# Kernel tuning notes

Measured on AMD Instinct MI355X. Metric: run time of the kernel, lower is better.

Reference implementation:

```python
import jax, jax.numpy as jnp
import numpy as np

N = 50000       # nodes
E = 800000      # edges (before self-loops)
F_IN = 128      # in_channels
HID = 32        # hidden_channels per head
HEADS = 4
OUT = 16        # out_channels
NEG_SLOPE = 0.2 # PyG GATConv leaky_relu slope
EPS = 1e-16     # PyG softmax denominator eps
BN_EPS = 1e-5


def setup_inputs() -> dict:
    key = jax.random.key(0)
    ks = jax.random.split(key, 20)
    rn = lambda k, shp, s=0.1: (jax.random.normal(k, shp, jnp.float32) * s)
    x = jax.random.normal(ks[0], (N, F_IN), jnp.float32)
    edge_index = jax.random.randint(ks[1], (2, E), 0, N, dtype=jnp.int32)
    D0 = HEADS * HID  # 128
    return {
        "x": x, "edge_index": edge_index,
        # layer 0: GATConv(F_IN -> HID, heads=HEADS, concat=True)
        "W0": rn(ks[2], (F_IN, HEADS * HID)), "as0": rn(ks[3], (HEADS, HID)),
        "ad0": rn(ks[4], (HEADS, HID)), "b0": jnp.zeros((D0,), jnp.float32),
        "g0": jnp.ones((D0,), jnp.float32) + rn(ks[5], (D0,), 0.05),
        "be0": rn(ks[6], (D0,), 0.05),
        # layer 1: GATConv(D0 -> HID, heads=HEADS, concat=True)
        "W1": rn(ks[7], (D0, HEADS * HID)), "as1": rn(ks[8], (HEADS, HID)),
        "ad1": rn(ks[9], (HEADS, HID)), "b1": jnp.zeros((D0,), jnp.float32),
        "g1": jnp.ones((D0,), jnp.float32) + rn(ks[10], (D0,), 0.05),
        "be1": rn(ks[11], (D0,), 0.05),
        # layer 2: GATConv(D0 -> OUT, heads=1, concat=False)
        "W2": rn(ks[12], (D0, OUT)), "as2": rn(ks[13], (1, OUT)),
        "ad2": rn(ks[14], (1, OUT)), "b2": jnp.zeros((OUT,), jnp.float32),
    }


def _gat(x, src, dst, W, a_s, a_d, b, heads, ch, concat):
    n = x.shape[0]
    h = (x @ W).reshape(n, heads, ch)                       # [N,H,C]
    score_s = (h * a_s).sum(-1)                             # [N,H]
    score_d = (h * a_d).sum(-1)                             # [N,H]
    e = jax.nn.leaky_relu(score_s[src] + score_d[dst], NEG_SLOPE)  # [E,H]
    emax = jax.ops.segment_max(e, dst, num_segments=n)
    emax = jnp.where(jnp.isfinite(emax), emax, 0.0)
    p = jnp.exp(e - emax[dst])
    denom = jax.ops.segment_sum(p, dst, num_segments=n)
    alpha = p / (denom[dst] + EPS)                          # segment softmax over dst
    out = jax.ops.segment_sum(h[src] * alpha[:, :, None], dst, num_segments=n)
    out = out.reshape(n, heads * ch) if concat else out.mean(axis=1)
    return out + b


def _bn(x, g, be):
    m = x.mean(0)
    v = x.var(0)
    return (x - m) * jax.lax.rsqrt(v + BN_EPS) * g + be


def reference(x, edge_index, W0, as0, ad0, b0, g0, be0,
              W1, as1, ad1, b1, g1, be1, W2, as2, ad2, b2):
    n = x.shape[0]
    loop = jnp.arange(n, dtype=edge_index.dtype)
    src = jnp.concatenate([edge_index[0], loop])  # PyG add_self_loops
    dst = jnp.concatenate([edge_index[1], loop])
    h = _gat(x, src, dst, W0, as0, ad0, b0, HEADS, HID, True)
    h = jax.nn.elu(_bn(h, g0, be0))                 # dropout disabled (eval)
    h = _gat(h, src, dst, W1, as1, ad1, b1, HEADS, HID, True)
    h = jax.nn.elu(_bn(h, g1, be1))
    return _gat(h, src, dst, W2, as2, ad2, b2, 1, OUT, False)
```

## Files before the change

kernel.cpp:

```cpp
#include <hip/hip_runtime.h>
#include <hip/hip_bf16.h>
#include <math.h>

#define NEG_SLOPE 0.2f
#define EPS_SM 1e-16f
#define BN_EPS 1e-5f
#define RANK_BLOCKS 256

typedef __attribute__((ext_vector_type(8))) short bf16x8;
typedef __attribute__((ext_vector_type(4))) float f32x4;

__device__ __forceinline__ float lrelu(float x) { return x > 0.f ? x : NEG_SLOPE * x; }
__device__ __forceinline__ ushort f2bf(float f) {
    uint u = __float_as_uint(f);
    return (ushort)((u + 0x7FFFu + ((u >> 16) & 1u)) >> 16);
}
__device__ __forceinline__ float bfl(uint u) { return __uint_as_float(u << 16); }
__device__ __forceinline__ float bfh(uint u) { return __uint_as_float(u & 0xFFFF0000u); }

__global__ void pack_w(const float* __restrict__ W0, const float* __restrict__ W1,
                       const float* __restrict__ W2, ushort* __restrict__ P0,
                       ushort* __restrict__ P1, ushort* __restrict__ P2) {
    int i = blockIdx.x * blockDim.x + threadIdx.x;
    const float* W;
    ushort* P;
    int NC, s;
    if (i < 16384) { W = W0; P = P0; NC = 128; s = i; }
    else if (i < 32768) { W = W1; P = P1; NC = 128; s = i - 16384; }
    else if (i < 34816) { W = W2; P = P2; NC = 16; s = i - 32768; }
    else return;
    int k = s / NC, col = s % NC;
    int CT = NC >> 4;
    int dst = (((k >> 5) * CT + (col >> 4)) << 9) +
              (((col & 15) | (((k >> 3) & 3) << 4)) << 3) + (k & 7);
    P[dst] = f2bf(W[s]);
}

template <int NC, bool BNELU, int HEADS, bool RANKFUSE>
__global__ __launch_bounds__(256) void gemm_mfma(
    const float* __restrict__ X, const ushort* __restrict__ Wp, ushort* __restrict__ Hb, int n,
    const float* __restrict__ sumsP, const float* __restrict__ g, const float* __restrict__ be,
    const float* __restrict__ as_, const float* __restrict__ ad_,
    float* __restrict__ ss, float* __restrict__ sd,
    const int* __restrict__ dstE, int E, int* __restrict__ deg, ushort* __restrict__ rank) {
    int tid = threadIdx.x;
    if constexpr (RANKFUSE) {
        if ((int)blockIdx.x < RANK_BLOCKS) {
            int T = RANK_BLOCKS * 256;
            for (int i = (int)blockIdx.x * 256 + tid; i < E; i += T)
                rank[i] = (ushort)atomicAdd(&deg[dstE[i]], 1);
            return;
        }
    }
    constexpr int CT = NC / 16;
    constexpr int FPH = NC / HEADS / 16;
    __shared__ __align__(16) ushort Xb[64 * 128];
    int bid = RANKFUSE ? ((int)blockIdx.x - RANK_BLOCKS) : (int)blockIdx.x;
    int row0 = bid * 64;
    float bnM[4], bnS[4], bnB[4];
    if constexpr (BNELU) {
        int c0 = (tid & 31) * 4;
        float inv_n = 1.f / (float)n;
#pragma unroll
        for (int j = 0; j < 4; ++j) {
            float m = sumsP[(c0 + j) * 16] * inv_n;
            float vv = fmaxf(sumsP[(128 + c0 + j) * 16] * inv_n - m * m, 0.f);
            bnM[j] = m;
            bnS[j] = rsqrtf(vv + BN_EPS) * g[c0 + j];
            bnB[j] = be[c0 + j];
        }
    }
#pragma unroll
    for (int i = 0; i < 8; ++i) {
        int idx = tid + i * 256;
        int row = idx >> 5, q = idx & 31;
        int gr = row0 + row;
        float4 v = make_float4(0.f, 0.f, 0.f, 0.f);
        if (gr < n) v = ((const float4*)(X + (long)gr * 128))[q];
        if constexpr (BNELU) {
            float y;
            y = (v.x - bnM[0]) * bnS[0] + bnB[0]; v.x = y > 0.f ? y : expm1f(y);
            y = (v.y - bnM[1]) * bnS[1] + bnB[1]; v.y = y > 0.f ? y : expm1f(y);
            y = (v.z - bnM[2]) * bnS[2] + bnB[2]; v.z = y > 0.f ? y : expm1f(y);
            y = (v.w - bnM[3]) * bnS[3] + bnB[3]; v.w = y > 0.f ? y : expm1f(y);
        }
        ushort4 p = make_ushort4(f2bf(v.x), f2bf(v.y), f2bf(v.z), f2bf(v.w));
        int s = (q >> 1) ^ (row & 15);
        *(ushort4*)&Xb[row * 128 + s * 8 + (q & 1) * 4] = p;
    }
    __syncthreads();
    int lane = tid & 63;
    int w = tid >> 6;
    int r0 = w * 16;
    int lrow = lane & 15, lhi = lane >> 4;
    f32x4 zero = {0.f, 0.f, 0.f, 0.f};
    f32x4 acc[CT];
#pragma unroll
    for (int f = 0; f < CT; ++f) acc[f] = zero;
    const ushort* xr = &Xb[(r0 + lrow) * 128];
#pragma unroll
    for (int ks = 0; ks < 4; ++ks) {
        int kg = ks * 4 + lhi;
        bf16x8 a = *(const bf16x8*)&xr[(kg ^ lrow) << 3];
#pragma unroll
        for (int f = 0; f < CT; ++f) {
            bf16x8 b = *(const bf16x8*)&Wp[((ks * CT + f) * 64 + lane) * 8];
            acc[f] = __builtin_amdgcn_mfma_f32_16x16x32_bf16(a, b, acc[f], 0, 0, 0);
        }
    }
    float asv[CT], adv[CT];
#pragma unroll
    for (int f = 0; f < CT; ++f) {
        asv[f] = as_[f * 16 + lrow];
        adv[f] = ad_[f * 16 + lrow];
    }
#pragma unroll
    for (int f = 0; f < CT; ++f)
#pragma unroll
        for (int j = 0; j < 4; ++j) {
            int gr = row0 + r0 + lhi * 4 + j;
            if (gr < n) Hb[(long)gr * NC + f * 16 + lrow] = f2bf(acc[f][j]);
        }
#pragma unroll
    for (int h = 0; h < HEADS; ++h) {
        float ps[4] = {}, pd[4] = {};
#pragma unroll
        for (int fi = 0; fi < FPH; ++fi) {
            int f = h * FPH + fi;
#pragma unroll
            for (int j = 0; j < 4; ++j) {
                ps[j] = fmaf(acc[f][j], asv[f], ps[j]);
                pd[j] = fmaf(acc[f][j], adv[f], pd[j]);
            }
        }
#pragma unroll
        for (int j = 0; j < 4; ++j) {
#pragma unroll
            for (int d = 1; d < 16; d <<= 1) {
                ps[j] += __shfl_xor(ps[j], d, 64);
                pd[j] += __shfl_xor(pd[j], d, 64);
            }
            int gr = row0 + r0 + lhi * 4 + j;
            if (lrow == 0 && gr < n) {
                ss[(long)gr * HEADS + h] = ps[j];
                sd[(long)gr * HEADS + h] = pd[j];
            }
        }
    }
}

__global__ __launch_bounds__(1024) void scan_kernel(const int* __restrict__ deg,
                                                    int* __restrict__ offs, int n) {
    __shared__ int wsum[16];
    __shared__ int wpre[16];
    __shared__ int carry_s;
    int tid = threadIdx.x;
    int lane = tid & 63;
    int w = tid >> 6;
    if (tid == 0) carry_s = 0;
    __syncthreads();
    int nv = (n + 3) >> 2;
    for (int base = 0; base < nv; base += 1024) {
        int carry = carry_s;
        int gi = base + tid;
        int e0 = gi * 4;
        int4 v = make_int4(0, 0, 0, 0);
        if (e0 + 3 < n) {
            v = ((const int4*)deg)[gi];
        } else if (e0 < n) {
            v.x = deg[e0];
            if (e0 + 1 < n) v.y = deg[e0 + 1];
            if (e0 + 2 < n) v.z = deg[e0 + 2];
        }
        int tsum = v.x + v.y + v.z + v.w;
        int incl = tsum;
#pragma unroll
        for (int d = 1; d < 64; d <<= 1) {
            int t = __shfl_up(incl, d, 64);
            if (lane >= d) incl += t;
        }
        if (lane == 63) wsum[w] = incl;
        __syncthreads();
        if (w == 0 && lane < 16) {
            int s = wsum[lane];
#pragma unroll
            for (int d = 1; d < 16; d <<= 1) {
                int t = __shfl_up(s, d, 64);
                if (lane >= d) s += t;
            }
            wpre[lane] = s;
        }
        __syncthreads();
        int wbase = (w == 0) ? 0 : wpre[w - 1];
        int ex = carry + wbase + incl - tsum;
        if (e0 < n) {
            int4 o;
            o.x = ex;
            o.y = ex + v.x;
            o.z = o.y + v.y;
            o.w = o.z + v.z;
            if (e0 + 3 < n) {
                ((int4*)offs)[gi] = o;
            } else {
                offs[e0] = o.x;
                if (e0 + 1 < n) offs[e0 + 1] = o.y;
                if (e0 + 2 < n) offs[e0 + 2] = o.z;
            }
        }
        __syncthreads();
        if (tid == 1023) carry_s = carry + wpre[15];
        __syncthreads();
    }
}

__global__ void scatter_kernel(const int* __restrict__ src, const int* __restrict__ dst,
                               const ushort* __restrict__ rank, const int* __restrict__ offs,
                               int E, int* __restrict__ srcs) {
    int i = blockIdx.x * blockDim.x + threadIdx.x;
    int T = gridDim.x * blockDim.x;
    for (; i < E; i += T) {
        int d = dst[i];
        srcs[offs[d] + (int)rank[i]] = src[i];
    }
}

__global__ __launch_bounds__(256) void gat_gather4(
    const uint* __restrict__ hb, const float* __restrict__ ss, const float* __restrict__ sd,
    const int* __restrict__ offs, const int* __restrict__ deg, const int* __restrict__ srcs,
    const float* __restrict__ bias, float* __restrict__ out, int n) {
    int wid = threadIdx.x >> 6;
    int lane = threadIdx.x & 63;
    int node = blockIdx.x * 4 + wid;
    if (node >= n) return;
    int off = offs[node];
    int dg = deg[node];
    int grp = lane >> 4;
    int ll = lane & 15;
    int hd = ll >> 2;
    float sdn = sd[node * 4 + hd];
    float es = lrelu(ss[node * 4 + hd] + sdn);
    const uint* hrow = hb + ll * 4;
    float acc[8] = {};
    float sm = 0.f;
#pragma unroll 2
    for (int i = grp; i < dg; i += 4) {
        int s = srcs[off + i];
        float w = __expf(lrelu(ss[s * 4 + hd] + sdn));
        sm += w;
        uint4 hv = *(const uint4*)(hrow + (long)s * 64);
        acc[0] = fmaf(w, bfl(hv.x), acc[0]);
        acc[1] = fmaf(w, bfh(hv.x), acc[1]);
        acc[2] = fmaf(w, bfl(hv.y), acc[2]);
        acc[3] = fmaf(w, bfh(hv.y), acc[3]);
        acc[4] = fmaf(w, bfl(hv.z), acc[4]);
        acc[5] = fmaf(w, bfh(hv.z), acc[5]);
        acc[6] = fmaf(w, bfl(hv.w), acc[6]);
        acc[7] = fmaf(w, bfh(hv.w), acc[7]);
    }
#pragma unroll
    for (int j = 0; j < 8; ++j) {
        acc[j] += __shfl_xor(acc[j], 16, 64);
        acc[j] += __shfl_xor(acc[j], 32, 64);
    }
    sm += __shfl_xor(sm, 16, 64);
    sm += __shfl_xor(sm, 32, 64);
    float wS = __expf(es);
    sm += wS;
    uint4 hvS = *(const uint4*)(hrow + (long)node * 64);
    acc[0] = fmaf(wS, bfl(hvS.x), acc[0]);
    acc[1] = fmaf(wS, bfh(hvS.x), acc[1]);
    acc[2] = fmaf(wS, bfl(hvS.y), acc[2]);
    acc[3] = fmaf(wS, bfh(hvS.y), acc[3]);
    acc[4] = fmaf(wS, bfl(hvS.z), acc[4]);
    acc[5] = fmaf(wS, bfh(hvS.z), acc[5]);
    acc[6] = fmaf(wS, bfl(hvS.w), acc[6]);
    acc[7] = fmaf(wS, bfh(hvS.w), acc[7]);
    float inv = 1.f / (sm + EPS_SM);
    if (grp == 0) {
        float4 bA = *(const float4*)&bias[ll * 8];
        float4 bB = *(const float4*)&bias[ll * 8 + 4];
        float4 o0 = make_float4(acc[0] * inv + bA.x, acc[1] * inv + bA.y,
                                acc[2] * inv + bA.z, acc[3] * inv + bA.w);
        float4 o1 = make_float4(acc[4] * inv + bB.x, acc[5] * inv + bB.y,
                                acc[6] * inv + bB.z, acc[7] * inv + bB.w);
        *(float4*)&out[(long)node * 128 + ll * 8] = o0;
        *(float4*)&out[(long)node * 128 + ll * 8 + 4] = o1;
    }
}

__global__ __launch_bounds__(256) void gat_gather1(
    const uint* __restrict__ hb2, const float* __restrict__ ss, const float* __restrict__ sd,
    const int* __restrict__ offs, const int* __restrict__ deg, const int* __restrict__ srcs,
    const float* __restrict__ bias, float* __restrict__ out, int n) {
    int wid = threadIdx.x >> 6;
    int lane = threadIdx.x & 63;
    int node = blockIdx.x * 4 + wid;
    if (node >= n) return;
    int off = offs[node];
    int dg = deg[node];
    int grp = lane >> 3;
    int ll = lane & 7;
    float sdn = sd[node];
    float es = lrelu(ss[node] + sdn);
    float a0 = 0.f, a1 = 0.f, sm = 0.f;
#pragma unroll 2
    for (int i = grp; i < dg; i += 8) {
        int s = srcs[off + i];
        float w = __expf(lrelu(ss[s] + sdn));
        sm += w;
        uint hv = hb2[s * 8 + ll];
        a0 = fmaf(w, bfl(hv), a0);
        a1 = fmaf(w, bfh(hv), a1);
    }
#pragma unroll
    for (int d = 8; d <= 32; d <<= 1) {
        a0 += __shfl_xor(a0, d, 64);
        a1 += __shfl_xor(a1, d, 64);
        sm += __shfl_xor(sm, d, 64);
    }
    float wS = __expf(es);
    sm += wS;
    uint hvS = hb2[node * 8 + ll];
    a0 = fmaf(wS, bfl(hvS), a0);
    a1 = fmaf(wS, bfh(hvS), a1);
    float inv = 1.f / (sm + EPS_SM);
    if (grp == 0) {
        float2 o = make_float2(a0 * inv + bias[ll * 2], a1 * inv + bias[ll * 2 + 1]);
        *(float2*)&out[(long)node * 16 + ll * 2] = o;
    }
}

__global__ __launch_bounds__(256) void bn_stats(const float* __restrict__ X,
                                                float* __restrict__ sumsP, int n) {
    __shared__ float red[2048];
    int tid = threadIdx.x;
    int q = tid & 31, r = tid >> 5;
    float s[4] = {}, s2[4] = {};
    long total4 = (long)n * 32;
    long T = (long)gridDim.x * 256;
    for (long i = (long)blockIdx.x * 256 + tid; i < total4; i += T) {
        float4 v = ((const float4*)X)[i];
        s[0] += v.x; s2[0] = fmaf(v.x, v.x, s2[0]);
        s[1] += v.y; s2[1] = fmaf(v.y, v.y, s2[1]);
        s[2] += v.z; s2[2] = fmaf(v.z, v.z, s2[2]);
        s[3] += v.w; s2[3] = fmaf(v.w, v.w, s2[3]);
    }
#pragma unroll
    for (int j = 0; j < 4; ++j) {
        red[(q * 8 + j) * 8 + r] = s[j];
        red[(q * 8 + 4 + j) * 8 + r] = s2[j];
    }
    __syncthreads();
    int ch = tid & 127, st = tid >> 7;
    int slot = (ch >> 2) * 8 + st * 4 + (ch & 3);
    float acc = 0.f;
#pragma unroll
    for (int rr = 0; rr < 8; ++rr) acc += red[slot * 8 + rr];
    atomicAdd(&sumsP[tid * 16], acc);
}

extern "C" void kernel_launch(void* const* d_in, const int* in_sizes, int n_in,
                              void* d_out, int out_size, void* d_ws, size_t ws_size,
                              hipStream_t stream) {
    const float* x = (const float*)d_in[0];
    const int* ei = (const int*)d_in[1];
    const float* W0 = (const float*)d_in[2];
    const float* as0 = (const float*)d_in[3];
    const float* ad0 = (const float*)d_in[4];
    const float* b0 = (const float*)d_in[5];
    const float* g0 = (const float*)d_in[6];
    const float* be0 = (const float*)d_in[7];
    const float* W1 = (const float*)d_in[8];
    const float* as1 = (const float*)d_in[9];
    const float* ad1 = (const float*)d_in[10];
    const float* b1 = (const float*)d_in[11];
    const float* g1 = (const float*)d_in[12];
    const float* be1 = (const float*)d_in[13];
    const float* W2 = (const float*)d_in[14];
    const float* as2 = (const float*)d_in[15];
    const float* ad2 = (const float*)d_in[16];
    const float* b2 = (const float*)d_in[17];

    int n = in_sizes[0] / 128;
    int E = in_sizes[1] / 2;
    const int* srcA = ei;
    const int* dstA = ei + E;

    char* base = (char*)d_ws;
    auto alloc = [&](size_t bytes) {
        char* p = base;
        base += (bytes + 255) & ~(size_t)255;
        return p;
    };
    ushort* hb = (ushort*)alloc((size_t)n * 128 * 2);
    float* act = (float*)alloc((size_t)n * 128 * 4);
    ushort* h2b = (ushort*)alloc((size_t)n * 16 * 2);
    float* ssb = (float*)alloc((size_t)n * 4 * 4);
    float* sdb = (float*)alloc((size_t)n * 4 * 4);
    float* sumsP0 = (float*)alloc(4096 * 4);
    float* sumsP1 = (float*)alloc(4096 * 4);
    int* deg = (int*)alloc((size_t)n * 4);
    int* offs = (int*)alloc((size_t)n * 4);
    ushort* rank = (ushort*)alloc((size_t)E * 2);
    int* srcs = (int*)alloc((size_t)E * 4);
    ushort* Wp0 = (ushort*)alloc(16384 * 2);
    ushort* Wp1 = (ushort*)alloc(16384 * 2);
    ushort* Wp2 = (ushort*)alloc(2048 * 2);

    float* out = (float*)d_out;

    hipMemsetAsync(deg, 0, (size_t)n * 4, stream);
    hipMemsetAsync(sumsP0, 0, 4096 * 4 * 2, stream);

    pack_w<<<136, 256, 0, stream>>>(W0, W1, W2, Wp0, Wp1, Wp2);

    int gGemm = (n + 63) / 64;
    int gWave = (n + 3) / 4;

    gemm_mfma<128, false, 4, true><<<RANK_BLOCKS + gGemm, 256, 0, stream>>>(
        x, Wp0, hb, n, nullptr, g0, be0, as0, ad0, ssb, sdb, dstA, E, deg, rank);
    scan_kernel<<<1, 1024, 0, stream>>>(deg, offs, n);
    scatter_kernel<<<2048, 256, 0, stream>>>(srcA, dstA, rank, offs, E, srcs);

    gat_gather4<<<gWave, 256, 0, stream>>>((const uint*)hb, ssb, sdb, offs, deg, srcs, b0, act, n);
    bn_stats<<<256, 256, 0, stream>>>(act, sumsP0, n);

    gemm_mfma<128, true, 4, false><<<gGemm, 256, 0, stream>>>(
        act, Wp1, hb, n, sumsP0, g0, be0, as1, ad1, ssb, sdb, nullptr, 0, nullptr, nullptr);
    gat_gather4<<<gWave, 256, 0, stream>>>((const uint*)hb, ssb, sdb, offs, deg, srcs, b1, act, n);
    bn_stats<<<256, 256, 0, stream>>>(act, sumsP1, n);

    gemm_mfma<16, true, 1, false><<<gGemm, 256, 0, stream>>>(
        act, Wp2, h2b, n, sumsP1, g1, be1, as2, ad2, ssb, sdb, nullptr, 0, nullptr, nullptr);
    gat_gather1<<<gWave, 256, 0, stream>>>((const uint*)h2b, ssb, sdb, offs, deg, srcs, b2, out, n);
}
```

Measured before the change: 243.9 us.

## Store intermediate activations in bf16 and stage GEMM outputs through LDS

Gather outputs of the first two GAT layers are now written as bf16 instead of fp32. BN stats and the BN+ELU GEMM prologue read bf16, which halves activation traffic. GEMM results and attention scores are staged in shared memory and written out with coalesced 16-byte stores instead of scattered 2-byte stores. RANK_BLOCKS is doubled. The trade-off is extra rounding of pre-BN activations to bf16, which slightly changes the BN statistics.

```diff
diff --git a/kernel.cpp b/kernel.cpp
--- a/kernel.cpp
+++ b/kernel.cpp
@@ -5,7 +5,7 @@
 #define NEG_SLOPE 0.2f
 #define EPS_SM 1e-16f
 #define BN_EPS 1e-5f
-#define RANK_BLOCKS 256
+#define RANK_BLOCKS 512
 
 typedef __attribute__((ext_vector_type(8))) short bf16x8;
 typedef __attribute__((ext_vector_type(4))) float f32x4;
@@ -36,11 +36,11 @@
     P[dst] = f2bf(W[s]);
 }
 
-template <int NC, bool BNELU, int HEADS, bool RANKFUSE>
+template <int NC, int HEADS, bool XBN, bool RANKFUSE>
 __global__ __launch_bounds__(256) void gemm_mfma(
-    const float* __restrict__ X, const ushort* __restrict__ Wp, ushort* __restrict__ Hb, int n,
-    const float* __restrict__ sumsP, const float* __restrict__ g, const float* __restrict__ be,
-    const float* __restrict__ as_, const float* __restrict__ ad_,
+    const void* __restrict__ Xv, const ushort* __restrict__ Wp, ushort* __restrict__ Hb,
+    int n, const float* __restrict__ sumsP, const float* __restrict__ g,
+    const float* __restrict__ be, const float* __restrict__ as_, const float* __restrict__ ad_,
     float* __restrict__ ss, float* __restrict__ sd,
     const int* __restrict__ dstE, int E, int* __restrict__ deg, ushort* __restrict__ rank) {
     int tid = threadIdx.x;
@@ -55,38 +55,55 @@
     constexpr int CT = NC / 16;
     constexpr int FPH = NC / HEADS / 16;
     __shared__ __align__(16) ushort Xb[64 * 128];
+    __shared__ float ssl[64 * HEADS], sdl[64 * HEADS];
     int bid = RANKFUSE ? ((int)blockIdx.x - RANK_BLOCKS) : (int)blockIdx.x;
     int row0 = bid * 64;
-    float bnM[4], bnS[4], bnB[4];
-    if constexpr (BNELU) {
-        int c0 = (tid & 31) * 4;
+    if constexpr (!XBN) {
+        const float* X = (const float*)Xv;
+#pragma unroll
+        for (int i = 0; i < 8; ++i) {
+            int idx = tid + i * 256;
+            int row = idx >> 5, q = idx & 31;
+            int gr = row0 + row;
+            float4 v = make_float4(0.f, 0.f, 0.f, 0.f);
+            if (gr < n) v = ((const float4*)(X + (long)gr * 128))[q];
+            ushort4 p = make_ushort4(f2bf(v.x), f2bf(v.y), f2bf(v.z), f2bf(v.w));
+            int s = (q >> 1) ^ (row & 15);
+            *(ushort4*)&Xb[row * 128 + s * 8 + (q & 1) * 4] = p;
+        }
+    } else {
+        const ushort* X = (const ushort*)Xv;
+        int c8 = (tid & 15) * 8;
         float inv_n = 1.f / (float)n;
-#pragma unroll
-        for (int j = 0; j < 4; ++j) {
-            float m = sumsP[(c0 + j) * 16] * inv_n;
-            float vv = fmaxf(sumsP[(128 + c0 + j) * 16] * inv_n - m * m, 0.f);
-            bnM[j] = m;
-            bnS[j] = rsqrtf(vv + BN_EPS) * g[c0 + j];
-            bnB[j] = be[c0 + j];
-        }
-    }
-#pragma unroll
-    for (int i = 0; i < 8; ++i) {
-        int idx = tid + i * 256;
-        int row = idx >> 5, q = idx & 31;
-        int gr = row0 + row;
-        float4 v = make_float4(0.f, 0.f, 0.f, 0.f);
-        if (gr < n) v = ((const float4*)(X + (long)gr * 128))[q];
-        if constexpr (BNELU) {
-            float y;
-            y = (v.x - bnM[0]) * bnS[0] + bnB[0]; v.x = y > 0.f ? y : expm1f(y);
-            y = (v.y - bnM[1]) * bnS[1] + bnB[1]; v.y = y > 0.f ? y : expm1f(y);
-            y = (v.z - bnM[2]) * bnS[2] + bnB[2]; v.z = y > 0.f ? y : expm1f(y);
-            y = (v.w - bnM[3]) * bnS[3] + bnB[3]; v.w = y > 0.f ? y : expm1f(y);
-        }
-        ushort4 p = make_ushort4(f2bf(v.x), f2bf(v.y), f2bf(v.z), f2bf(v.w));
-        int s = (q >> 1) ^ (row & 15);
-        *(ushort4*)&Xb[row * 128 + s * 8 + (q & 1) * 4] = p;
+        float bm[8], bs[8], bb[8];
+#pragma unroll
+        for (int j = 0; j < 8; ++j) {
+            int ch = c8 + j;
+            float m = sumsP[ch * 16] * inv_n;
+            float vv = fmaxf(sumsP[(128 + ch) * 16] * inv_n - m * m, 0.f);
+            bm[j] = m;
+            bs[j] = rsqrtf(vv + BN_EPS) * g[ch];
+            bb[j] = be[ch];
+        }
+#pragma unroll
+        for (int i = 0; i < 4; ++i) {
+            int idx = tid + i * 256;
+            int row = idx >> 4, g8 = idx & 15;
+            int gr = row0 + row;
+            uint4 v = make_uint4(0, 0, 0, 0);
+            if (gr < n) v = ((const uint4*)(X + (long)gr * 128))[g8];
+            float a, b;
+#define BNE(comp, j0)                                                  \
+    a = bfl(comp); b = bfh(comp);                                      \
+    a = (a - bm[j0]) * bs[j0] + bb[j0]; a = a > 0.f ? a : expm1f(a);   \
+    b = (b - bm[j0 + 1]) * bs[j0 + 1] + bb[j0 + 1];                    \
+    b = b > 0.f ? b : expm1f(b);                                       \
+    comp = (uint)f2bf(a) | ((uint)f2bf(b) << 16);
+            BNE(v.x, 0) BNE(v.y, 2) BNE(v.z, 4) BNE(v.w, 6)
+#undef BNE
+            int s = g8 ^ (row & 15);
+            *(uint4*)&Xb[row * 128 + s * 8] = v;
+        }
     }
     __syncthreads();
     int lane = tid & 63;
@@ -108,19 +125,18 @@
             acc[f] = __builtin_amdgcn_mfma_f32_16x16x32_bf16(a, b, acc[f], 0, 0, 0);
         }
     }
+    __syncthreads();
+#pragma unroll
+    for (int f = 0; f < CT; ++f)
+#pragma unroll
+        for (int j = 0; j < 4; ++j)
+            Xb[(r0 + lhi * 4 + j) * NC + f * 16 + lrow] = f2bf(acc[f][j]);
     float asv[CT], adv[CT];
 #pragma unroll
     for (int f = 0; f < CT; ++f) {
         asv[f] = as_[f * 16 + lrow];
         adv[f] = ad_[f * 16 + lrow];
     }
-#pragma unroll
-    for (int f = 0; f < CT; ++f)
-#pragma unroll
-        for (int j = 0; j < 4; ++j) {
-            int gr = row0 + r0 + lhi * 4 + j;
-            if (gr < n) Hb[(long)gr * NC + f * 16 + lrow] = f2bf(acc[f][j]);
-        }
 #pragma unroll
     for (int h = 0; h < HEADS; ++h) {
         float ps[4] = {}, pd[4] = {};
@@ -140,11 +156,29 @@
                 ps[j] += __shfl_xor(ps[j], d, 64);
                 pd[j] += __shfl_xor(pd[j], d, 64);
             }
-            int gr = row0 + r0 + lhi * 4 + j;
-            if (lrow == 0 && gr < n) {
-                ss[(long)gr * HEADS + h] = ps[j];
-                sd[(long)gr * HEADS + h] = pd[j];
+            if (lrow == 0) {
+                ssl[(r0 + lhi * 4 + j) * HEADS + h] = ps[j];
+                sdl[(r0 + lhi * 4 + j) * HEADS + h] = pd[j];
             }
+        }
+    }
+    __syncthreads();
+    constexpr int NU = 64 * NC / 8;
+#pragma unroll
+    for (int i = 0; i < (NU + 255) / 256; ++i) {
+        int idx = tid + i * 256;
+        if (idx < NU) {
+            int row = idx / (NC / 8), c8i = idx % (NC / 8);
+            int gr = row0 + row;
+            if (gr < n) ((uint4*)&Hb[(long)gr * NC])[c8i] = ((const uint4*)Xb)[idx];
+        }
+    }
+    if (tid < 64 * HEADS) {
+        int row = tid / HEADS, hh = tid % HEADS;
+        int gr = row0 + row;
+        if (gr < n) {
+            ss[(long)gr * HEADS + hh] = ssl[tid];
+            sd[(long)gr * HEADS + hh] = sdl[tid];
         }
     }
 }
@@ -227,7 +261,7 @@
 __global__ __launch_bounds__(256) void gat_gather4(
     const uint* __restrict__ hb, const float* __restrict__ ss, const float* __restrict__ sd,
     const int* __restrict__ offs, const int* __restrict__ deg, const int* __restrict__ srcs,
-    const float* __restrict__ bias, float* __restrict__ out, int n) {
+    const float* __restrict__ bias, ushort* __restrict__ outb, int n) {
     int wid = threadIdx.x >> 6;
     int lane = threadIdx.x & 63;
     int node = blockIdx.x * 4 + wid;
@@ -279,12 +313,12 @@
     if (grp == 0) {
         float4 bA = *(const float4*)&bias[ll * 8];
         float4 bB = *(const float4*)&bias[ll * 8 + 4];
-        float4 o0 = make_float4(acc[0] * inv + bA.x, acc[1] * inv + bA.y,
-                                acc[2] * inv + bA.z, acc[3] * inv + bA.w);
-        float4 o1 = make_float4(acc[4] * inv + bB.x, acc[5] * inv + bB.y,
-                                acc[6] * inv + bB.z, acc[7] * inv + bB.w);
-        *(float4*)&out[(long)node * 128 + ll * 8] = o0;
-        *(float4*)&out[(long)node * 128 + ll * 8 + 4] = o1;
+        uint4 p;
+        p.x = (uint)f2bf(acc[0] * inv + bA.x) | ((uint)f2bf(acc[1] * inv + bA.y) << 16);
+        p.y = (uint)f2bf(acc[2] * inv + bA.z) | ((uint)f2bf(acc[3] * inv + bA.w) << 16);
+        p.z = (uint)f2bf(acc[4] * inv + bB.x) | ((uint)f2bf(acc[5] * inv + bB.y) << 16);
+        p.w = (uint)f2bf(acc[6] * inv + bB.z) | ((uint)f2bf(acc[7] * inv + bB.w) << 16);
+        *(uint4*)&outb[(long)node * 128 + ll * 8] = p;
     }
 }
 
@@ -330,33 +364,37 @@
     }
 }
 
-__global__ __launch_bounds__(256) void bn_stats(const float* __restrict__ X,
-                                                float* __restrict__ sumsP, int n) {
-    __shared__ float red[2048];
+__global__ __launch_bounds__(256) void bn_stats_bf16(const uint4* __restrict__ X4,
+                                                     float* __restrict__ sumsP, int n) {
+    __shared__ float red[4096];
     int tid = threadIdx.x;
-    int q = tid & 31, r = tid >> 5;
-    float s[4] = {}, s2[4] = {};
-    long total4 = (long)n * 32;
+    float s[8] = {}, s2[8] = {};
+    long tot = (long)n * 16;
     long T = (long)gridDim.x * 256;
-    for (long i = (long)blockIdx.x * 256 + tid; i < total4; i += T) {
-        float4 v = ((const float4*)X)[i];
-        s[0] += v.x; s2[0] = fmaf(v.x, v.x, s2[0]);
-        s[1] += v.y; s2[1] = fmaf(v.y, v.y, s2[1]);
-        s[2] += v.z; s2[2] = fmaf(v.z, v.z, s2[2]);
-        s[3] += v.w; s2[3] = fmaf(v.w, v.w, s2[3]);
-    }
-#pragma unroll
-    for (int j = 0; j < 4; ++j) {
-        red[(q * 8 + j) * 8 + r] = s[j];
-        red[(q * 8 + 4 + j) * 8 + r] = s2[j];
+    for (long i = (long)blockIdx.x * 256 + tid; i < tot; i += T) {
+        uint4 v = X4[i];
+        float f;
+        f = bfl(v.x); s[0] += f; s2[0] = fmaf(f, f, s2[0]);
+        f = bfh(v.x); s[1] += f; s2[1] = fmaf(f, f, s2[1]);
+        f = bfl(v.y); s[2] += f; s2[2] = fmaf(f, f, s2[2]);
+        f = bfh(v.y); s[3] += f; s2[3] = fmaf(f, f, s2[3]);
+        f = bfl(v.z); s[4] += f; s2[4] = fmaf(f, f, s2[4]);
+        f = bfh(v.z); s[5] += f; s2[5] = fmaf(f, f, s2[5]);
+        f = bfl(v.w); s[6] += f; s2[6] = fmaf(f, f, s2[6]);
+        f = bfh(v.w); s[7] += f; s2[7] = fmaf(f, f, s2[7]);
+    }
+#pragma unroll
+    for (int j = 0; j < 8; ++j) {
+        red[j * 256 + tid] = s[j];
+        red[(8 + j) * 256 + tid] = s2[j];
     }
     __syncthreads();
     int ch = tid & 127, st = tid >> 7;
-    int slot = (ch >> 2) * 8 + st * 4 + (ch & 3);
-    float acc = 0.f;
-#pragma unroll
-    for (int rr = 0; rr < 8; ++rr) acc += red[slot * 8 + rr];
-    atomicAdd(&sumsP[tid * 16], acc);
+    int base = (st * 8 + (ch & 7)) * 256 + (ch >> 3);
+    float a = 0.f;
+#pragma unroll
+    for (int rep = 0; rep < 16; ++rep) a += red[base + rep * 16];
+    atomicAdd(&sumsP[tid * 16], a);
 }
 
 extern "C" void kernel_launch(void* const* d_in, const int* in_sizes, int n_in,
@@ -393,7 +431,7 @@
         return p;
     };
     ushort* hb = (ushort*)alloc((size_t)n * 128 * 2);
-    float* act = (float*)alloc((size_t)n * 128 * 4);
+    ushort* actb = (ushort*)alloc((size_t)n * 128 * 2);
     ushort* h2b = (ushort*)alloc((size_t)n * 16 * 2);
     float* ssb = (float*)alloc((size_t)n * 4 * 4);
     float* sdb = (float*)alloc((size_t)n * 4 * 4);
@@ -417,20 +455,20 @@
     int gGemm = (n + 63) / 64;
     int gWave = (n + 3) / 4;
 
-    gemm_mfma<128, false, 4, true><<<RANK_BLOCKS + gGemm, 256, 0, stream>>>(
+    gemm_mfma<128, 4, false, true><<<RANK_BLOCKS + gGemm, 256, 0, stream>>>(
         x, Wp0, hb, n, nullptr, g0, be0, as0, ad0, ssb, sdb, dstA, E, deg, rank);
     scan_kernel<<<1, 1024, 0, stream>>>(deg, offs, n);
     scatter_kernel<<<2048, 256, 0, stream>>>(srcA, dstA, rank, offs, E, srcs);
 
-    gat_gather4<<<gWave, 256, 0, stream>>>((const uint*)hb, ssb, sdb, offs, deg, srcs, b0, act, n);
-    bn_stats<<<256, 256, 0, stream>>>(act, sumsP0, n);
-
-    gemm_mfma<128, true, 4, false><<<gGemm, 256, 0, stream>>>(
-        act, Wp1, hb, n, sumsP0, g0, be0, as1, ad1, ssb, sdb, nullptr, 0, nullptr, nullptr);
-    gat_gather4<<<gWave, 256, 0, stream>>>((const uint*)hb, ssb, sdb, offs, deg, srcs, b1, act, n);
-    bn_stats<<<256, 256, 0, stream>>>(act, sumsP1, n);
-
-    gemm_mfma<16, true, 1, false><<<gGemm, 256, 0, stream>>>(
-        act, Wp2, h2b, n, sumsP1, g1, be1, as2, ad2, ssb, sdb, nullptr, 0, nullptr, nullptr);
+    gat_gather4<<<gWave, 256, 0, stream>>>((const uint*)hb, ssb, sdb, offs, deg, srcs, b0, actb, n);
+    bn_stats_bf16<<<256, 256, 0, stream>>>((const uint4*)actb, sumsP0, n);
+
+    gemm_mfma<128, 4, true, false><<<gGemm, 256, 0, stream>>>(
+        actb, Wp1, hb, n, sumsP0, g0, be0, as1, ad1, ssb, sdb, nullptr, 0, nullptr, nullptr);
+    gat_gather4<<<gWave, 256, 0, stream>>>((const uint*)hb, ssb, sdb, offs, deg, srcs, b1, actb, n);
+    bn_stats_bf16<<<256, 256, 0, stream>>>((const uint4*)actb, sumsP1, n);
+
+    gemm_mfma<16, 1, true, false><<<gGemm, 256, 0, stream>>>(
+        actb, Wp2, h2b, n, sumsP1, g1, be1, as2, ad2, ssb, sdb, nullptr, 0, nullptr, nullptr);
     gat_gather1<<<gWave, 256, 0, stream>>>((const uint*)h2b, ssb, sdb, offs, deg, srcs, b2, out, n);
 }
```

Measured after the change: 242.8 us. About the same (-0.4%).
